# Optimization experiments

Hardware: AMD Instinct MI355X
Metric: run time of the kernel (lower is better)

Reference implementation:

```python
import jax, jax.numpy as jnp
import numpy as np

N_NODES = 50000
N_EDGES = 400000
D = 64          # in/out channels (residual forces equality)
H = 8           # attention heads
L = 3           # number of GATv2 layers
NEG_SLOPE = 0.2
LN_EPS = 1e-5


def setup_inputs() -> dict:
    key = jax.random.key(0)
    ks = jax.random.split(key, 6)
    x = jax.random.normal(ks[0], (N_NODES, D), dtype=jnp.float32)
    edge_index = jax.random.randint(ks[1], (2, N_EDGES), 0, N_NODES, dtype=jnp.int64)
    scale = 1.0 / np.sqrt(D)
    Wl = jax.random.normal(ks[2], (L, D, H * D), dtype=jnp.float32) * scale
    Wr = jax.random.normal(ks[3], (L, D, H * D), dtype=jnp.float32) * scale
    att = jax.random.normal(ks[4], (L, H, D), dtype=jnp.float32) * 0.1
    b = jnp.zeros((L, D), dtype=jnp.float32)
    gamma = jnp.ones((L, D), dtype=jnp.float32)
    beta = jnp.zeros((L, D), dtype=jnp.float32)
    return {"x": x, "Wl": Wl, "Wr": Wr, "att": att, "b": b,
            "gamma": gamma, "beta": beta, "edge_index": edge_index}


def _gatv2_stack(x, Wl, Wr, att, b, gamma, beta, src, dst, num_nodes):
    # src/dst already include self-loops (PyG add_self_loops=True)
    for l in range(Wl.shape[0]):
        xl = (x @ Wl[l]).reshape(num_nodes, H, -1)   # [N,H,C] messages (source transform)
        xr = (x @ Wr[l]).reshape(num_nodes, H, -1)   # [N,H,C] target transform
        m = jax.nn.leaky_relu(xl[src] + xr[dst], NEG_SLOPE)       # [E,H,C]
        e = jnp.einsum('ehc,hc->eh', m, att[l])                    # [E,H]
        # segment softmax over incoming edges of each target node
        emax = jax.ops.segment_max(e, dst, num_segments=num_nodes)
        ex = jnp.exp(e - emax[dst])
        denom = jax.ops.segment_sum(ex, dst, num_segments=num_nodes)
        alpha = ex / denom[dst]                                    # [E,H]
        agg = jax.ops.segment_sum(alpha[:, :, None] * xl[src], dst,
                                  num_segments=num_nodes)          # [N,H,C]
        h = agg.mean(axis=1) + b[l]                                # concat=False -> head mean, + bias
        x = h + x                                                  # residual
        mu = x.mean(-1, keepdims=True)
        var = x.var(-1, keepdims=True)
        x = (x - mu) / jnp.sqrt(var + LN_EPS) * gamma[l] + beta[l] # LayerNorm
        x = jax.nn.relu(x)
    return x


def reference(x, Wl, Wr, att, b, gamma, beta, edge_index):
    num_nodes = x.shape[0]
    loops = jnp.arange(num_nodes, dtype=edge_index.dtype)
    src = jnp.concatenate([edge_index[0], loops])
    dst = jnp.concatenate([edge_index[1], loops])
    return _gatv2_stack(x, Wl, Wr, att, b, gamma, beta, src, dst, num_nodes)
```

## Files before the change

### kernel.cpp

```cpp
#include <hip/hip_runtime.h>

#define N_NODES 50000
#define N_EDGES 400000
#define EP (N_EDGES + N_NODES)
#define D 64
#define H 8
#define NEG_SLOPE 0.2f
#define LN_EPS 1e-5f
#define CHUNK 196
#define SCAN_BLOCKS 256
#define PAD_N 50048
#define GEMM_BLOCKS (782 * 8)
#define LOG2E 1.4426950408889634f

typedef unsigned short ushort_t;
typedef unsigned int uint_t;
typedef unsigned char uchar_t;
typedef __attribute__((ext_vector_type(8))) short short8;
typedef __attribute__((ext_vector_type(4))) float f32x4;
typedef __attribute__((ext_vector_type(2))) float f32x2;

#if defined(__has_builtin)
#if __has_builtin(__builtin_amdgcn_cvt_pk_bf16_f32)
#define HAVE_CVT_PK_BF16 1
#endif
#endif

__device__ __forceinline__ ushort_t f2bf(float f) {
    uint_t u = __float_as_uint(f);
    u += 0x7fffu + ((u >> 16) & 1u);
    return (ushort_t)(u >> 16);
}
__device__ __forceinline__ uint_t pack_bf2(float a, float b) {
#ifdef HAVE_CVT_PK_BF16
    typedef __attribute__((ext_vector_type(2))) __bf16 bf16x2_t;
    bf16x2_t v = __builtin_amdgcn_cvt_pk_bf16_f32(a, b);
    uint_t r;
    __builtin_memcpy(&r, &v, 4);
    return r;
#else
    return (uint_t)f2bf(a) | ((uint_t)f2bf(b) << 16);
#endif
}
__device__ __forceinline__ f32x2 mkf2(uint_t u) {
    f32x2 r;
    r.x = __uint_as_float(u << 16);
    r.y = __uint_as_float(u & 0xffff0000u);
    return r;
}
template <bool HI>
__device__ __forceinline__ f32x2 cvt8(uint_t u) {
    typedef __attribute__((ext_vector_type(2))) float v2f;
    v2f r = __builtin_amdgcn_cvt_pk_f32_fp8((int)u, HI);
    return (f32x2){r.x, r.y};
}

__device__ __forceinline__ f32x2 pk_add(f32x2 a, f32x2 b) {
    f32x2 d;
    asm("v_pk_add_f32 %0, %1, %2" : "=v"(d) : "v"(a), "v"(b));
    return d;
}
__device__ __forceinline__ f32x2 pk_mul(f32x2 a, f32x2 b) {
    f32x2 d;
    asm("v_pk_mul_f32 %0, %1, %2" : "=v"(d) : "v"(a), "v"(b));
    return d;
}
__device__ __forceinline__ f32x2 pk_fma(f32x2 a, f32x2 b, f32x2 c) {
    f32x2 d;
    asm("v_pk_fma_f32 %0, %1, %2, %3" : "=v"(d) : "v"(a), "v"(b), "v"(c));
    return d;
}
__device__ __forceinline__ f32x2 pk_abs(f32x2 a) {
    f32x2 r;
    r.x = __uint_as_float(__float_as_uint(a.x) & 0x7fffffffu);
    r.y = __uint_as_float(__float_as_uint(a.y) & 0x7fffffffu);
    return r;
}

__device__ __forceinline__ float xor1_dpp(float x) {
    int i = __float_as_int(x);
    return __int_as_float(__builtin_amdgcn_update_dpp(i, i, 0xB1, 0xF, 0xF, 1));
}
__device__ __forceinline__ float xor2_dpp(float x) {
    int i = __float_as_int(x);
    return __int_as_float(__builtin_amdgcn_update_dpp(i, i, 0x4E, 0xF, 0xF, 1));
}
__device__ __forceinline__ float xor8_dpp(float x) {
    int i = __float_as_int(x);
    return __int_as_float(__builtin_amdgcn_update_dpp(i, i, 0x128, 0xF, 0xF, 1));
}
__device__ __forceinline__ float xor4_swz(float x) {
    return __int_as_float(__builtin_amdgcn_ds_swizzle(__float_as_int(x), 0x101F));
}
__device__ __forceinline__ float xor16_swz(float x) {
    return __int_as_float(__builtin_amdgcn_ds_swizzle(__float_as_int(x), 0x401F));
}

__device__ __forceinline__ void edge_sd(const int* __restrict__ ei, int eid, int& s, int& d) {
    if (eid < N_EDGES) { s = ei[eid]; d = ei[N_EDGES + eid]; }
    else               { s = d = eid - N_EDGES; }
}


__global__ __launch_bounds__(256) void setup_all(const int* __restrict__ ei, int* __restrict__ counts,
                                                 const float* __restrict__ x,
                                                 const float* __restrict__ Wl, const float* __restrict__ Wr,
                                                 ushort_t* __restrict__ xb, ushort_t* __restrict__ Wt) {
    int t = blockIdx.x * 256 + threadIdx.x;
    if (t < EP) {
        int s, d; edge_sd(ei, t, s, d);
        atomicAdd(&counts[d], 1);
        return;
    }
    t -= EP;
    if (t < N_NODES * 64) { xb[t] = f2bf(x[t]); return; }
    t -= N_NODES * 64;
    if (t >= 3 * 1024 * 64) return;
    int l = t >> 16, rem = t & 65535, col = rem >> 6, k = rem & 63;
    float v = (col < 512) ? Wl[((size_t)l * 64 + k) * 512 + col]
                          : Wr[((size_t)l * 64 + k) * 512 + (col - 512)];
    Wt[t] = f2bf(v);
}


__global__ __launch_bounds__(256) void csr_scan1(const int* __restrict__ counts, int* __restrict__ bsum,
                                                 int* __restrict__ bhist) {
    __shared__ int sd[256];
    __shared__ int hist[64];
    int t = threadIdx.x, b = blockIdx.x;
    if (t < 64) hist[t] = 0;
    int idx = b * CHUNK + t;
    int v = (t < CHUNK && idx < N_NODES) ? counts[idx] : 0;
    sd[t] = v;
    __syncthreads();
    if (t < CHUNK && idx < N_NODES) atomicAdd(&hist[63 - min(v, 63)], 1);
    for (int d = 128; d > 0; d >>= 1) {
        __syncthreads();
        if (t < d) sd[t] += sd[t + d];
    }
    __syncthreads();
    if (t == 0) bsum[b] = sd[0];
    if (t < 64) bhist[b * 64 + t] = hist[t];
}

__global__ __launch_bounds__(256) void csr_scan2(int* __restrict__ bsum,
                                                 const int* __restrict__ bhist, int* __restrict__ pbase) {
    __shared__ int sd[256];
    __shared__ int sg[64 * 4];
    __shared__ int base[64];
    int t = threadIdx.x;
    sd[t] = bsum[t];
    __syncthreads();
    for (int d = 1; d < 256; d <<= 1) {
        int v = (t >= d) ? sd[t - d] : 0;
        __syncthreads();
        if (t >= d) sd[t] += v;
        __syncthreads();
    }
    bsum[t] = (t > 0) ? sd[t - 1] : 0;

    int k = t & 63, g = t >> 6;
    int s = 0;
    for (int j = 0; j < 64; ++j) s += bhist[(g * 64 + j) * 64 + k];
    sg[k * 4 + g] = s;
    __syncthreads();
    if (t == 0) {
        int run = 0;
        for (int kk = 0; kk < 64; ++kk) {
            base[kk] = run;
            run += sg[kk * 4 + 0] + sg[kk * 4 + 1] + sg[kk * 4 + 2] + sg[kk * 4 + 3];
        }
    }
    __syncthreads();
    int run = base[k];
    for (int gg = 0; gg < g; ++gg) run += sg[k * 4 + gg];
    for (int j = 0; j < 64; ++j) {
        int b = g * 64 + j;
        pbase[b * 64 + k] = run;
        run += bhist[b * 64 + k];
    }
}

__global__ __launch_bounds__(256) void csr_scan3(const int* __restrict__ counts, const int* __restrict__ bsum,
                                                 int* __restrict__ cursor,
                                                 const int* __restrict__ pbase, int4* __restrict__ desc) {
    __shared__ int sd[256];
    __shared__ int cur[64];
    int t = threadIdx.x, b = blockIdx.x;
    if (t < 64) cur[t] = pbase[b * 64 + t];
    int idx = b * CHUNK + t;
    int v = (t < CHUNK && idx < N_NODES) ? counts[idx] : 0;
    sd[t] = v;
    __syncthreads();
    for (int d = 1; d < 256; d <<= 1) {
        int u = (t >= d) ? sd[t - d] : 0;
        __syncthreads();
        if (t >= d) sd[t] += u;
        __syncthreads();
    }
    if (t < CHUNK && idx < N_NODES) {
        int ex = bsum[b] + sd[t] - v;
        cursor[idx] = ex;
        int bin = 63 - min(v, 63);
        int p = atomicAdd(&cur[bin], 1);
        desc[p] = make_int4(idx, ex, ex + v, 0);
    }
}

__global__ __launch_bounds__(256) void gemm_mfma(const ushort_t* __restrict__ xb,
                                                 const ushort_t* __restrict__ Wt,
                                                 uchar_t* __restrict__ x8,
                                                 const int* __restrict__ ei, int* __restrict__ cursor,
                                                 int* __restrict__ csr_src) {
    __shared__ ushort_t sW[128 * 72];
    __shared__ uchar_t sOut[64 * 144];
    int b = blockIdx.x;
    if (b >= GEMM_BLOCKS) {
        int t = (b - GEMM_BLOCKS) * 256 + threadIdx.x;
        if (t >= EP) return;
        int s, d; edge_sd(ei, t, s, d);
        int pos = atomicAdd(&cursor[d], 1);
        csr_src[pos] = s;
        return;
    }
    int colq = b / 782;
    int bx = b - colq * 782;
    int t = threadIdx.x;
    const ushort_t* Wg = Wt + (size_t)colq * 128 * 64;
    {
        int col = t >> 1, half = t & 1;
        const uint4* g = (const uint4*)(Wg + col * 64 + half * 32);
        uint4* l = (uint4*)(sW + col * 72 + half * 32);
        l[0] = g[0]; l[1] = g[1]; l[2] = g[2]; l[3] = g[3];
    }
    __syncthreads();
    int lane = t & 63, w = t >> 6;
    int ln = lane & 15, q = lane >> 4;
    int nl = w * 16 + ln;
    int node = bx * 64 + nl;
    int nclamp = node < N_NODES ? node : N_NODES - 1;
    const short8 b0 = *(const short8*)(xb + (size_t)nclamp * 64 + q * 8);
    const short8 b1 = *(const short8*)(xb + (size_t)nclamp * 64 + 32 + q * 8);
#pragma unroll
    for (int ct = 0; ct < 8; ++ct) {
        const short8 a0 = *(const short8*)(sW + (ct * 16 + ln) * 72 + q * 8);
        const short8 a1 = *(const short8*)(sW + (ct * 16 + ln) * 72 + 32 + q * 8);
        f32x4 acc = {0.f, 0.f, 0.f, 0.f};
        acc = __builtin_amdgcn_mfma_f32_16x16x32_bf16(a0, b0, acc, 0, 0, 0);
        acc = __builtin_amdgcn_mfma_f32_16x16x32_bf16(a1, b1, acc, 0, 0, 0);
        int r = 0;
        r = __builtin_amdgcn_cvt_pk_fp8_f32(acc[0], acc[1], r, false);
        r = __builtin_amdgcn_cvt_pk_fp8_f32(acc[2], acc[3], r, true);
        *(uint_t*)(sOut + nl * 144 + ct * 16 + q * 4) = (uint_t)r;
    }
    __syncthreads();
#pragma unroll
    for (int k = 0; k < 2; ++k) {
        int c = t + k * 256;
        int nl2 = c >> 3, off = (c & 7) * 16;
        int node2 = bx * 64 + nl2;
        if (node2 < N_NODES) {
            uint4 v = *(const uint4*)(sOut + nl2 * 144 + off);
            *(uint4*)(x8 + (size_t)node2 * 1024 + colq * 128 + off) = v;
        }
    }
}

__global__ __launch_bounds__(256, 8) void node_fused(ushort_t* __restrict__ xb,
                                                  const uchar_t* __restrict__ x8,
                                                  const float* __restrict__ att,
                                                  const int4* __restrict__ desc, const int* __restrict__ csr_src,
                                                  const float* __restrict__ bias, const float* __restrict__ gamma,
                                                  const float* __restrict__ beta, float* __restrict__ x_out,
                                                  int write_out, int write_xb) {
    int4 dd = desc[blockIdx.x * 4 + (threadIdx.x >> 6)];
    int n   = __builtin_amdgcn_readfirstlane(dd.x);
    int beg = __builtin_amdgcn_readfirstlane(dd.y);
    int end = __builtin_amdgcn_readfirstlane(dd.z);
    int lane = threadIdx.x & 63;
    int h = lane >> 3, i = lane & 7;
    int off8 = h * 64 + i * 8;

    uint2 ru = *(const uint2*)(x8 + (size_t)n * 1024 + 512 + off8);
    f32x2 rv0 = cvt8<false>(ru.x), rv1 = cvt8<true>(ru.x),
          rv2 = cvt8<false>(ru.y), rv3 = cvt8<true>(ru.y);
    const float4* pa = (const float4*)(att + h * 64 + i * 8);
    float4 aa = pa[0], ab = pa[1];
    f32x2 a0 = {aa.x, aa.y}, a1 = {aa.z, aa.w}, a2 = {ab.x, ab.y}, a3 = {ab.z, ab.w};
    f32x2 a60 = (0.6f * LOG2E) * a0, a61 = (0.6f * LOG2E) * a1,
          a62 = (0.6f * LOG2E) * a2, a63 = (0.6f * LOG2E) * a3;
    f32x2 a40 = (0.4f * LOG2E) * a0, a41 = (0.4f * LOG2E) * a1,
          a42 = (0.4f * LOG2E) * a2, a43 = (0.4f * LOG2E) * a3;

    float den = 0.f;
    f32x2 acc0 = {0.f, 0.f}, acc1 = {0.f, 0.f}, acc2 = {0.f, 0.f}, acc3 = {0.f, 0.f};

#define PROCESS(cur)                                                     \
    {                                                                    \
        f32x2 v0 = cvt8<false>(cur.x), v1 = cvt8<true>(cur.x),           \
              v2 = cvt8<false>(cur.y), v3 = cvt8<true>(cur.y);           \
        f32x2 p = pk_mul(a60, v0);                                       \
        p = pk_fma(a61, v1, p);                                          \
        p = pk_fma(a62, v2, p);                                          \
        p = pk_fma(a63, v3, p);                                          \
        p = pk_fma(a40, pk_abs(pk_add(v0, rv0)), p);                     \
        p = pk_fma(a41, pk_abs(pk_add(v1, rv1)), p);                     \
        p = pk_fma(a42, pk_abs(pk_add(v2, rv2)), p);                     \
        p = pk_fma(a43, pk_abs(pk_add(v3, rv3)), p);                     \
        float pdot = p.x + p.y;                                          \
        pdot += xor1_dpp(pdot);                                          \
        pdot += xor2_dpp(pdot);                                          \
        pdot += xor4_swz(pdot);                                          \
        float wgt = __builtin_exp2f(pdot);                               \
        den += wgt;                                                      \
        f32x2 wv = {wgt, wgt};                                           \
        acc0 = pk_fma(wv, v0, acc0);                                     \
        acc1 = pk_fma(wv, v1, acc1);                                     \
        acc2 = pk_fma(wv, v2, acc2);                                     \
        acc3 = pk_fma(wv, v3, acc3);                                     \
    }

    for (int base = beg; base < end; base += 64) {
        int idx = base + lane;
        int srcs = csr_src[idx < end ? idx : end - 1];
        int cnt = min(64, end - base);
        int j = 0;
        for (; j + 8 <= cnt; j += 8) {
            uint2 q[8];
#pragma unroll
            for (int u = 0; u < 8; ++u) {
                int ss = __shfl(srcs, j + u);
                q[u] = *(const uint2*)(x8 + (size_t)ss * 1024 + off8);
            }
#pragma unroll
            for (int u = 0; u < 8; ++u) PROCESS(q[u]);
        }
        for (; j < cnt; ++j) {
            int ss = __shfl(srcs, j);
            uint2 qq = *(const uint2*)(x8 + (size_t)ss * 1024 + off8);
            PROCESS(qq);
        }
    }
#undef PROCESS

    float invden = 0.125f / den;
    f32x2 iv = {invden, invden};
    acc0 = pk_mul(acc0, iv); acc1 = pk_mul(acc1, iv);
    acc2 = pk_mul(acc2, iv); acc3 = pk_mul(acc3, iv);
    float acc[8] = {acc0.x, acc0.y, acc1.x, acc1.y, acc2.x, acc2.y, acc3.x, acc3.y};
#pragma unroll
    for (int k2 = 0; k2 < 8; ++k2) {
        acc[k2] += xor8_dpp(acc[k2]);
        acc[k2] += xor16_swz(acc[k2]);
        acc[k2] += __shfl_xor(acc[k2], 32);
    }

    int cbase = i * 8;
    uint4 pxu = *(const uint4*)(xb + (size_t)n * 64 + cbase);
    f32x2 x01 = mkf2(pxu.x), x23 = mkf2(pxu.y), x45 = mkf2(pxu.z), x67 = mkf2(pxu.w);
    float xi[8] = {x01.x, x01.y, x23.x, x23.y, x45.x, x45.y, x67.x, x67.y};
    float v[8];
    float sum = 0.f, sq = 0.f;
#pragma unroll
    for (int k2 = 0; k2 < 8; ++k2) {
        float val = acc[k2] + bias[cbase + k2] + xi[k2];
        v[k2] = val; sum += val; sq += val * val;
    }
    sum += xor1_dpp(sum); sq += xor1_dpp(sq);
    sum += xor2_dpp(sum); sq += xor2_dpp(sq);
    sum += xor4_swz(sum); sq += xor4_swz(sq);
    float mu   = sum * (1.0f / 64.0f);
    float var  = sq * (1.0f / 64.0f) - mu * mu;
    float rstd = rsqrtf(var + LN_EPS);

    if (h == 0) {
        float o[8];
#pragma unroll
        for (int k2 = 0; k2 < 8; ++k2) {
            float y = (v[k2] - mu) * rstd * gamma[cbase + k2] + beta[cbase + k2];
            o[k2] = fmaxf(y, 0.f);
        }
        if (write_out) {
            float4* po = (float4*)(x_out + n * 64 + cbase);
            po[0] = make_float4(o[0], o[1], o[2], o[3]);
            po[1] = make_float4(o[4], o[5], o[6], o[7]);
        }
        if (write_xb) {
            *(uint4*)(xb + (size_t)n * 64 + cbase) =
                make_uint4(pack_bf2(o[0], o[1]), pack_bf2(o[2], o[3]),
                           pack_bf2(o[4], o[5]), pack_bf2(o[6], o[7]));
        }
    }
}


extern "C" void kernel_launch(void* const* d_in, const int* in_sizes, int n_in,
                              void* d_out, int out_size, void* d_ws, size_t ws_size,
                              hipStream_t stream) {
    const float* x     = (const float*)d_in[0];
    const float* Wl    = (const float*)d_in[1];
    const float* Wr    = (const float*)d_in[2];
    const float* att   = (const float*)d_in[3];
    const float* b     = (const float*)d_in[4];
    const float* gamma = (const float*)d_in[5];
    const float* beta  = (const float*)d_in[6];
    const int*   ei    = (const int*)d_in[7];
    float* out = (float*)d_out;

    uchar_t* x8    = (uchar_t*)d_ws;
    ushort_t* xb   = (ushort_t*)(x8 + (size_t)PAD_N * 1024);
    ushort_t* Wt   = xb + (size_t)PAD_N * 64;
    int* counts    = (int*)(Wt + 3 * 1024 * 64);
    int* cursor    = counts + PAD_N;
    int* bsum      = cursor + PAD_N;
    int* bhist     = bsum + 256;
    int* pbase     = bhist + SCAN_BLOCKS * 64;
    int4* desc     = (int4*)(pbase + SCAN_BLOCKS * 64);
    int* csr_src   = (int*)(desc + PAD_N);

    hipMemsetAsync(counts, 0, N_NODES * sizeof(int), stream);

    int setup_threads = EP + N_NODES * 64 + 3 * 1024 * 64;
    setup_all<<<(setup_threads + 255) / 256, 256, 0, stream>>>(ei, counts, x, Wl, Wr, xb, Wt);

    csr_scan1<<<SCAN_BLOCKS, 256, 0, stream>>>(counts, bsum, bhist);
    csr_scan2<<<1, 256, 0, stream>>>(bsum, bhist, pbase);
    csr_scan3<<<SCAN_BLOCKS, 256, 0, stream>>>(counts, bsum, cursor, pbase, desc);

    int eb = (EP + 255) / 256;
    for (int l = 0; l < 3; ++l) {
        int grid = (l == 0) ? GEMM_BLOCKS + eb : GEMM_BLOCKS;
        gemm_mfma <<<grid, 256, 0, stream>>>(xb, Wt + (size_t)l * 1024 * 64, x8, ei, cursor, csr_src);
        node_fused<<<N_NODES / 4, 256, 0, stream>>>(xb, x8, att + l * (H * D), desc, csr_src,
                                                    b + l * D, gamma + l * D, beta + l * D,
                                                    out, (l == 2) ? 1 : 0, (l < 2) ? 1 : 0);
    }
}
```

Baseline: 385.3 us.

## Fuse setup and CSR scan kernels into one persistent kernel with grid barriers

Result: slower. 510.7 us (+32.6%).

```diff
diff --git a/kernel.cpp b/kernel.cpp
--- a/kernel.cpp
+++ b/kernel.cpp
@@ -101,109 +101,121 @@
     else               { s = d = eid - N_EDGES; }
 }
 
-
-__global__ __launch_bounds__(256) void setup_all(const int* __restrict__ ei, int* __restrict__ counts,
-                                                 const float* __restrict__ x,
-                                                 const float* __restrict__ Wl, const float* __restrict__ Wr,
-                                                 ushort_t* __restrict__ xb, ushort_t* __restrict__ Wt) {
-    int t = blockIdx.x * 256 + threadIdx.x;
-    if (t < EP) {
-        int s, d; edge_sd(ei, t, s, d);
-        atomicAdd(&counts[d], 1);
-        return;
-    }
-    t -= EP;
-    if (t < N_NODES * 64) { xb[t] = f2bf(x[t]); return; }
-    t -= N_NODES * 64;
-    if (t >= 3 * 1024 * 64) return;
-    int l = t >> 16, rem = t & 65535, col = rem >> 6, k = rem & 63;
-    float v = (col < 512) ? Wl[((size_t)l * 64 + k) * 512 + col]
-                          : Wr[((size_t)l * 64 + k) * 512 + (col - 512)];
-    Wt[t] = f2bf(v);
-}
-
-
-__global__ __launch_bounds__(256) void csr_scan1(const int* __restrict__ counts, int* __restrict__ bsum,
-                                                 int* __restrict__ bhist) {
-    __shared__ int sd[256];
-    __shared__ int hist[64];
-    int t = threadIdx.x, b = blockIdx.x;
-    if (t < 64) hist[t] = 0;
-    int idx = b * CHUNK + t;
-    int v = (t < CHUNK && idx < N_NODES) ? counts[idx] : 0;
-    sd[t] = v;
+__device__ __forceinline__ void gbar(int* ctr, int nblk) {
     __syncthreads();
-    if (t < CHUNK && idx < N_NODES) atomicAdd(&hist[63 - min(v, 63)], 1);
-    for (int d = 128; d > 0; d >>= 1) {
-        __syncthreads();
-        if (t < d) sd[t] += sd[t + d];
+    if (threadIdx.x == 0) {
+        __threadfence();
+        atomicAdd(ctr, 1);
+        while (__hip_atomic_load(ctr, __ATOMIC_ACQUIRE, __HIP_MEMORY_SCOPE_AGENT) < nblk) {}
+        __threadfence();
     }
     __syncthreads();
-    if (t == 0) bsum[b] = sd[0];
-    if (t < 64) bhist[b * 64 + t] = hist[t];
-}
-
-__global__ __launch_bounds__(256) void csr_scan2(int* __restrict__ bsum,
-                                                 const int* __restrict__ bhist, int* __restrict__ pbase) {
-    __shared__ int sd[256];
-    __shared__ int sg[64 * 4];
-    __shared__ int base[64];
-    int t = threadIdx.x;
-    sd[t] = bsum[t];
-    __syncthreads();
-    for (int d = 1; d < 256; d <<= 1) {
-        int v = (t >= d) ? sd[t - d] : 0;
-        __syncthreads();
-        if (t >= d) sd[t] += v;
-        __syncthreads();
-    }
-    bsum[t] = (t > 0) ? sd[t - 1] : 0;
-
-    int k = t & 63, g = t >> 6;
-    int s = 0;
-    for (int j = 0; j < 64; ++j) s += bhist[(g * 64 + j) * 64 + k];
-    sg[k * 4 + g] = s;
-    __syncthreads();
-    if (t == 0) {
-        int run = 0;
-        for (int kk = 0; kk < 64; ++kk) {
-            base[kk] = run;
-            run += sg[kk * 4 + 0] + sg[kk * 4 + 1] + sg[kk * 4 + 2] + sg[kk * 4 + 3];
-        }
-    }
-    __syncthreads();
-    int run = base[k];
-    for (int gg = 0; gg < g; ++gg) run += sg[k * 4 + gg];
-    for (int j = 0; j < 64; ++j) {
-        int b = g * 64 + j;
-        pbase[b * 64 + k] = run;
-        run += bhist[b * 64 + k];
-    }
-}
-
-__global__ __launch_bounds__(256) void csr_scan3(const int* __restrict__ counts, const int* __restrict__ bsum,
-                                                 int* __restrict__ cursor,
-                                                 const int* __restrict__ pbase, int4* __restrict__ desc) {
-    __shared__ int sd[256];
-    __shared__ int cur[64];
-    int t = threadIdx.x, b = blockIdx.x;
-    if (t < 64) cur[t] = pbase[b * 64 + t];
-    int idx = b * CHUNK + t;
-    int v = (t < CHUNK && idx < N_NODES) ? counts[idx] : 0;
-    sd[t] = v;
-    __syncthreads();
-    for (int d = 1; d < 256; d <<= 1) {
-        int u = (t >= d) ? sd[t - d] : 0;
-        __syncthreads();
-        if (t >= d) sd[t] += u;
-        __syncthreads();
-    }
-    if (t < CHUNK && idx < N_NODES) {
-        int ex = bsum[b] + sd[t] - v;
-        cursor[idx] = ex;
-        int bin = 63 - min(v, 63);
-        int p = atomicAdd(&cur[bin], 1);
-        desc[p] = make_int4(idx, ex, ex + v, 0);
+}
+
+__global__ __launch_bounds__(256) void fused_setup(const int* __restrict__ ei, int* __restrict__ counts,
+                                                   const float* __restrict__ x,
+                                                   const float* __restrict__ Wl, const float* __restrict__ Wr,
+                                                   ushort_t* __restrict__ xb, ushort_t* __restrict__ Wt,
+                                                   int* __restrict__ bsum, int* __restrict__ bhist,
+                                                   int* __restrict__ pbase, int* __restrict__ cursor,
+                                                   int4* __restrict__ desc, int* __restrict__ bar) {
+    int b = blockIdx.x, t = threadIdx.x;
+
+    const int T1 = EP + N_NODES * 64 + 3 * 1024 * 64;
+    for (int g = b * 256 + t; g < T1; g += SCAN_BLOCKS * 256) {
+        int w = g;
+        if (w < EP) {
+            int s, d; edge_sd(ei, w, s, d);
+            atomicAdd(&counts[d], 1);
+            continue;
+        }
+        w -= EP;
+        if (w < N_NODES * 64) { xb[w] = f2bf(x[w]); continue; }
+        w -= N_NODES * 64;
+        int l = w >> 16, rem = w & 65535, col = rem >> 6, k = rem & 63;
+        float v = (col < 512) ? Wl[((size_t)l * 64 + k) * 512 + col]
+                              : Wr[((size_t)l * 64 + k) * 512 + (col - 512)];
+        Wt[w] = f2bf(v);
+    }
+    gbar(&bar[0], SCAN_BLOCKS);
+
+    {
+        __shared__ int sd[256];
+        __shared__ int hist[64];
+        if (t < 64) hist[t] = 0;
+        int idx = b * CHUNK + t;
+        int v = (t < CHUNK && idx < N_NODES) ? counts[idx] : 0;
+        sd[t] = v;
+        __syncthreads();
+        if (t < CHUNK && idx < N_NODES) atomicAdd(&hist[63 - min(v, 63)], 1);
+        for (int d = 128; d > 0; d >>= 1) {
+            __syncthreads();
+            if (t < d) sd[t] += sd[t + d];
+        }
+        __syncthreads();
+        if (t == 0) bsum[b] = sd[0];
+        if (t < 64) bhist[b * 64 + t] = hist[t];
+    }
+    gbar(&bar[1], SCAN_BLOCKS);
+
+    if (b == 0) {
+        __shared__ int sd[256];
+        __shared__ int sg[64 * 4];
+        __shared__ int base[64];
+        sd[t] = bsum[t];
+        __syncthreads();
+        for (int d = 1; d < 256; d <<= 1) {
+            int v = (t >= d) ? sd[t - d] : 0;
+            __syncthreads();
+            if (t >= d) sd[t] += v;
+            __syncthreads();
+        }
+        bsum[t] = (t > 0) ? sd[t - 1] : 0;
+
+        int k = t & 63, g = t >> 6;
+        int s = 0;
+        for (int j = 0; j < 64; ++j) s += bhist[(g * 64 + j) * 64 + k];
+        sg[k * 4 + g] = s;
+        __syncthreads();
+        if (t == 0) {
+            int run = 0;
+            for (int kk = 0; kk < 64; ++kk) {
+                base[kk] = run;
+                run += sg[kk * 4 + 0] + sg[kk * 4 + 1] + sg[kk * 4 + 2] + sg[kk * 4 + 3];
+            }
+        }
+        __syncthreads();
+        int run = base[k];
+        for (int gg = 0; gg < g; ++gg) run += sg[k * 4 + gg];
+        for (int j = 0; j < 64; ++j) {
+            int bb = g * 64 + j;
+            pbase[bb * 64 + k] = run;
+            run += bhist[bb * 64 + k];
+        }
+    }
+    gbar(&bar[2], SCAN_BLOCKS);
+
+    {
+        __shared__ int sd[256];
+        __shared__ int cur[64];
+        if (t < 64) cur[t] = pbase[b * 64 + t];
+        int idx = b * CHUNK + t;
+        int v = (t < CHUNK && idx < N_NODES) ? counts[idx] : 0;
+        sd[t] = v;
+        __syncthreads();
+        for (int d = 1; d < 256; d <<= 1) {
+            int u = (t >= d) ? sd[t - d] : 0;
+            __syncthreads();
+            if (t >= d) sd[t] += u;
+            __syncthreads();
+        }
+        if (t < CHUNK && idx < N_NODES) {
+            int ex = bsum[b] + sd[t] - v;
+            cursor[idx] = ex;
+            int bin = 63 - min(v, 63);
+            int p = atomicAdd(&cur[bin], 1);
+            desc[p] = make_int4(idx, ex, ex + v, 0);
+        }
     }
 }
 
@@ -411,21 +423,18 @@
     ushort_t* xb   = (ushort_t*)(x8 + (size_t)PAD_N * 1024);
     ushort_t* Wt   = xb + (size_t)PAD_N * 64;
     int* counts    = (int*)(Wt + 3 * 1024 * 64);
-    int* cursor    = counts + PAD_N;
+    int* bar       = counts + PAD_N;
+    int* cursor    = bar + 8;
     int* bsum      = cursor + PAD_N;
     int* bhist     = bsum + 256;
     int* pbase     = bhist + SCAN_BLOCKS * 64;
     int4* desc     = (int4*)(pbase + SCAN_BLOCKS * 64);
     int* csr_src   = (int*)(desc + PAD_N);
 
-    hipMemsetAsync(counts, 0, N_NODES * sizeof(int), stream);
-
-    int setup_threads = EP + N_NODES * 64 + 3 * 1024 * 64;
-    setup_all<<<(setup_threads + 255) / 256, 256, 0, stream>>>(ei, counts, x, Wl, Wr, xb, Wt);
-
-    csr_scan1<<<SCAN_BLOCKS, 256, 0, stream>>>(counts, bsum, bhist);
-    csr_scan2<<<1, 256, 0, stream>>>(bsum, bhist, pbase);
-    csr_scan3<<<SCAN_BLOCKS, 256, 0, stream>>>(counts, bsum, cursor, pbase, desc);
+    hipMemsetAsync(counts, 0, (PAD_N + 8) * sizeof(int), stream);
+
+    fused_setup<<<SCAN_BLOCKS, 256, 0, stream>>>(ei, counts, x, Wl, Wr, xb, Wt,
+                                                 bsum, bhist, pbase, cursor, desc, bar);
 
     int eb = (EP + 255) / 256;
     for (int l = 0; l < 3; ++l) {
```
